# Performance work log

Hardware: AMD Instinct MI355X
Metric: run time of the kernel (lower is better)

The kernel has to match this reference:

```python
import jax, jax.numpy as jnp
import numpy as np

N = 100000       # num nodes
E = 1000000      # num edges
D_IN = 128       # input feature dim
D_H = 64         # hidden = output dim
EPS = 1e-5       # GraphNorm eps
SLOPE = 0.2      # LeakyReLU negative slope


def _glorot(key, shape):
    lim = float(np.sqrt(6.0 / (shape[0] + shape[1])))
    return jax.random.uniform(key, shape, jnp.float32, -lim, lim)


def setup_inputs() -> dict:
    key = jax.random.key(0)
    ks = jax.random.split(key, 6)
    return {
        "x": jax.random.normal(ks[0], (N, D_IN), jnp.float32),
        "edge_index": jax.random.randint(ks[1], (2, E), 0, N),
        "W_in": _glorot(ks[2], (D_IN, D_H)),
        "b_in": jnp.zeros((D_H,), jnp.float32),
        "W1": _glorot(ks[3], (D_H, D_H)),
        "b1": jnp.zeros((D_H,), jnp.float32),
        "gn1_alpha": jnp.ones((D_H,), jnp.float32),
        "gn1_gamma": jnp.ones((D_H,), jnp.float32),
        "gn1_beta": jnp.zeros((D_H,), jnp.float32),
        "W2": _glorot(ks[4], (D_H, D_H)),
        "b2": jnp.zeros((D_H,), jnp.float32),
        "gn2_alpha": jnp.ones((D_H,), jnp.float32),
        "gn2_gamma": jnp.ones((D_H,), jnp.float32),
        "gn2_beta": jnp.zeros((D_H,), jnp.float32),
    }


def gcn_conv(x, W, b, src, dst):
    # GCNConv with added self-loops and symmetric normalization:
    # out = D^{-1/2} (A + I) D^{-1/2} (x W) + b
    xw = x @ W                                                 # [N, D]
    ones = jnp.ones((src.shape[0],), x.dtype)
    deg = jax.ops.segment_sum(ones, dst, num_segments=x.shape[0]) + 1.0  # +1 self-loop
    dinv = jax.lax.rsqrt(deg)                                  # [N]
    coef = dinv[src] * dinv[dst]                               # [E]
    agg = jax.ops.segment_sum(xw[src] * coef[:, None], dst, num_segments=x.shape[0])
    return agg + xw * (dinv * dinv)[:, None] + b


def graph_norm(x, alpha, gamma, beta):
    # PyG GraphNorm over a single graph: per-feature mean/var over all nodes
    mean = jnp.mean(x, axis=0)
    c = x - alpha * mean
    var = jnp.mean(c * c, axis=0)
    return gamma * c * jax.lax.rsqrt(var + EPS) + beta


def reference(x, edge_index, W_in, b_in, W1, b1, gn1_alpha, gn1_gamma, gn1_beta,
              W2, b2, gn2_alpha, gn2_gamma, gn2_beta):
    src, dst = edge_index[0], edge_index[1]
    h = x @ W_in + b_in                                        # input projection
    h = graph_norm(gcn_conv(h, W1, b1, src, dst), gn1_alpha, gn1_gamma, gn1_beta)
    h = jnp.where(h > 0, h, SLOPE * h)                         # LeakyReLU(0.2); dropout=eval (identity)
    h = graph_norm(gcn_conv(h, W2, b2, src, dst), gn2_alpha, gn2_gamma, gn2_beta)
    return h                                                    # [N, D_H]
```

## Files before the change

kernel.cpp:

```cpp
#include <hip/hip_runtime.h>
#include <stdint.h>

#define N_NODES 100000
#define N_EDGES 1000000
#define D_IN 128
#define D_H 64
#define EPS 1e-5f
#define SLOPE 0.2f

typedef unsigned short u16;
typedef unsigned int u32;
typedef __attribute__((ext_vector_type(8))) short bf16x8;
typedef __attribute__((ext_vector_type(4))) float f32x4;

__device__ __forceinline__ float bf2f(u16 u) {
    union { u32 i; float f; } v; v.i = ((u32)u) << 16; return v.f;
}
__device__ __forceinline__ u16 f2bf(float f) {
    union { float f; u32 i; } v; v.f = f;
    u32 r = (v.i + 0x7fffu + ((v.i >> 16) & 1u)) >> 16;
    return (u16)r;
}
__device__ __forceinline__ bool is_f32(const void* flagp) {
    return *(const u32*)flagp == 0x3F800000u;
}
__device__ __forceinline__ float loadf(const void* p, size_t i, bool m) {
    return m ? ((const float*)p)[i] : bf2f(((const u16*)p)[i]);
}

__global__ __launch_bounds__(256) void kpf(const void* __restrict__ W_in,
                     const void* __restrict__ b_in,
                     const void* __restrict__ W1, const void* __restrict__ W2,
                     const void* __restrict__ flagp, const int* __restrict__ ei,
                     u16* __restrict__ WcT, u16* __restrict__ W2T,
                     float* __restrict__ bc, u16* __restrict__ xwb_pad,
                     int* __restrict__ cnt, int* __restrict__ bucket16,
                     int* __restrict__ ovf)
{
    bool m = is_f32(flagp);
    int t = threadIdx.x;
    int bid = blockIdx.x;
    if (bid < 64) {
        int c = bid;
        __shared__ float w1c[D_H];
        if (t < D_H) w1c[t] = loadf(W1, t * D_H + c, m);
        __syncthreads();
        if (t < D_IN) {
            float acc = 0.f;
            #pragma unroll 8
            for (int j = 0; j < D_H; j++) acc += loadf(W_in, t * D_H + j, m) * w1c[j];
            WcT[c * D_IN + t] = f2bf(acc);
        }
        if (t == 0) {
            float b = 0.f;
            for (int j = 0; j < D_H; j++) b += loadf(b_in, j, m) * w1c[j];
            bc[c] = b;
        }
        if (c == 0 && t < D_H) xwb_pad[(size_t)N_NODES * D_H + t] = 0;
    } else if (bid < 80) {
        int idx = (bid - 64) * 256 + t;
        int n = idx >> 6, k = idx & 63;
        W2T[n * D_H + k] = f2bf(loadf(W2, k * D_H + n, m));
    } else {
        int e4 = (bid - 80) * 1024 + t * 4;
        if (e4 < N_EDGES) {
            int4 s4 = *(const int4*)(ei + e4);
            int4 d4 = *(const int4*)(ei + N_EDGES + e4);
            int ss[4] = {s4.x, s4.y, s4.z, s4.w};
            int dd[4] = {d4.x, d4.y, d4.z, d4.w};
            #pragma unroll
            for (int j = 0; j < 4; j++) {
                int slot = atomicAdd(&cnt[dd[j]], 1);
                if (slot < 16)      bucket16[(size_t)dd[j] * 16 + slot] = ss[j];
                else if (slot < 64) ovf[(size_t)dd[j] * 48 + slot - 16] = ss[j];
            }
        }
    }
}

__global__ __launch_bounds__(256) void kgemm1(const void* __restrict__ x,
        const u16* __restrict__ WcT, const float* __restrict__ bc,
        const int* __restrict__ cnt, const void* __restrict__ flagp,
        u16* __restrict__ xwb)
{
    bool m = is_f32(flagp);
    __shared__ __align__(16) u16 xs[64 * 136];
    __shared__ __align__(16) u16 WT[64 * 136];
    int tid = threadIdx.x;
    int row0 = blockIdx.x * 64;
    for (int i = tid; i < 64 * 32; i += 256) {
        int r = i >> 5, kq = (i & 31) * 4;
        *(ushort4*)(WT + r * 136 + kq) = *(const ushort4*)(WcT + r * D_IN + kq);
    }
    for (int i = tid; i < 64 * 32; i += 256) {
        int r = i >> 5, kq = (i & 31) * 4;
        int gr = row0 + r;
        ushort4 u = make_ushort4(0, 0, 0, 0);
        if (gr < N_NODES) {
            if (m) {
                float4 v = *(const float4*)((const float*)x + (size_t)gr * D_IN + kq);
                u = make_ushort4(f2bf(v.x), f2bf(v.y), f2bf(v.z), f2bf(v.w));
            } else {
                u = *(const ushort4*)((const u16*)x + (size_t)gr * D_IN + kq);
            }
        }
        *(ushort4*)(xs + r * 136 + kq) = u;
    }
    __syncthreads();
    int w = tid >> 6, L = tid & 63;
    int q = L >> 4, c = L & 15;
    f32x4 acc[4];
    #pragma unroll
    for (int ct = 0; ct < 4; ct++) {
        float b = bc[ct * 16 + c];
        acc[ct] = (f32x4){b, b, b, b};
    }
    const u16* ap = xs + (w * 16 + c) * 136 + q * 8;
    #pragma unroll
    for (int kk = 0; kk < 4; kk++) {
        bf16x8 af = *(const bf16x8*)(ap + kk * 32);
        #pragma unroll
        for (int ct = 0; ct < 4; ct++) {
            bf16x8 bfr = *(const bf16x8*)(WT + (ct * 16 + c) * 136 + kk * 32 + q * 8);
            acc[ct] = __builtin_amdgcn_mfma_f32_16x16x32_bf16(af, bfr, acc[ct], 0, 0, 0);
        }
    }
    #pragma unroll
    for (int r = 0; r < 4; r++) {
        int gr = row0 + w * 16 + q * 4 + r;
        if (gr < N_NODES) {
            float ds = rsqrtf((float)cnt[gr] + 1.0f);
            #pragma unroll
            for (int ct = 0; ct < 4; ct++)
                xwb[(size_t)gr * D_H + ct * 16 + c] = f2bf(acc[ct][r] * ds);
        }
    }
}

__global__ __launch_bounds__(256) void kagg(const u16* __restrict__ xwb,
        const int* __restrict__ cnt, const int* __restrict__ bucket16,
        const int* __restrict__ ovf, const void* __restrict__ bvec,
        const void* __restrict__ flagp,
        u16* __restrict__ ybuf, float* __restrict__ accum)
{
    bool m = is_f32(flagp);
    __shared__ float red_s[4][64], red_q[4][64];
    int tid = threadIdx.x;
    int wv = tid >> 6, L = tid & 63;
    int half = L >> 5, mm = L & 31;
    int node0 = blockIdx.x * 32 + wv * 8;

    int cnt8 = cnt[node0 + (L & 7)];
    int tl = L >> 4, sl = L & 15;
    int raw0 = bucket16[(size_t)(node0 + tl) * 16 + sl];
    int raw1 = bucket16[(size_t)(node0 + 4 + tl) * 16 + sl];

    float b0 = loadf(bvec, 2 * mm, m), b1 = loadf(bvec, 2 * mm + 1, m);
    float ls0 = 0, ls1 = 0, lq0 = 0, lq1 = 0;

    const char* xb = (const char*)xwb;
    u32 moff = (u32)(mm << 2);

    auto srcof = [&](int g, int s, int degn, int ng) -> u32 {
        int rw = __shfl((g < 2) ? raw0 : raw1, (((g & 1) * 2 + half) << 4) + s);
        int sv = (s < degn) ? rw : ((s == degn) ? ng : N_NODES);
        return ((u32)sv << 7) | moff;
    };

    int cvg = __shfl(cnt8, half);
    int degn = min(cvg, 64);
    int ng = node0 + half;
    u32 cur[16];
    #pragma unroll
    for (int s = 0; s < 16; s++)
        cur[s] = *(const u32*)(xb + srcof(0, s, degn, ng));

    #pragma unroll
    for (int g = 0; g < 4; g++) {
        u32 nxt[16];
        int cvn = 0, degx = 0, ngx = 0;
        if (g < 3) {
            cvn = __shfl(cnt8, 2 * (g + 1) + half);
            degx = min(cvn, 64);
            ngx = node0 + 2 * (g + 1) + half;
            #pragma unroll
            for (int s = 0; s < 16; s++)
                nxt[s] = *(const u32*)(xb + srcof(g + 1, s, degx, ngx));
        }
        float a0 = 0.f, a1 = 0.f;
        #pragma unroll
        for (int s = 0; s < 16; s++) {
            a0 += __uint_as_float(cur[s] << 16);
            a1 += __uint_as_float(cur[s] & 0xffff0000u);
        }
        if (degn >= 16) {
            for (int s = 16; s <= degn; s++) {
                int sv = (s < degn) ? ovf[(size_t)ng * 48 + s - 16] : ng;
                u32 v = *(const u32*)(xb + (((u32)sv << 7) | moff));
                a0 += __uint_as_float(v << 16);
                a1 += __uint_as_float(v & 0xffff0000u);
            }
        }
        float ddn = rsqrtf((float)cvg + 1.0f);
        float y0 = ddn * a0 + b0;
        float y1 = ddn * a1 + b1;
        ((u32*)(ybuf + (size_t)ng * D_H))[mm] = (u32)f2bf(y0) | ((u32)f2bf(y1) << 16);
        ls0 += y0; ls1 += y1; lq0 += y0 * y0; lq1 += y1 * y1;
        #pragma unroll
        for (int s = 0; s < 16; s++) cur[s] = nxt[s];
        cvg = cvn; degn = degx; ng = ngx;
    }

    ls0 += __shfl_xor(ls0, 32); ls1 += __shfl_xor(ls1, 32);
    lq0 += __shfl_xor(lq0, 32); lq1 += __shfl_xor(lq1, 32);
    if (half == 0) {
        *(float2*)&red_s[wv][2 * mm] = make_float2(ls0, ls1);
        *(float2*)&red_q[wv][2 * mm] = make_float2(lq0, lq1);
    }
    __syncthreads();
    if (tid < 64) {
        atomicAdd(&accum[tid],      red_s[0][tid] + red_s[1][tid] + red_s[2][tid] + red_s[3][tid]);
        atomicAdd(&accum[64 + tid], red_q[0][tid] + red_q[1][tid] + red_q[2][tid] + red_q[3][tid]);
    }
}

__global__ __launch_bounds__(256) void kgemm2(const u16* __restrict__ y1b,
        const u16* __restrict__ W2T, const float* __restrict__ accum,
        const void* __restrict__ alpha, const void* __restrict__ gamma,
        const void* __restrict__ beta, const void* __restrict__ flagp,
        const int* __restrict__ cnt, u16* __restrict__ xwb)
{
    bool m = is_f32(flagp);
    __shared__ __align__(16) u16 hs[64 * 72];
    __shared__ __align__(16) u16 WT[64 * 72];
    __shared__ float aL[64], cL[64];
    int tid = threadIdx.x;
    if (tid < 64) {
        float mean = accum[tid] * (1.0f / N_NODES);
        float al = loadf(alpha, tid, m);
        float var = accum[64 + tid] * (1.0f / N_NODES) - mean * mean * al * (2.0f - al);
        var = fmaxf(var, 0.f);
        float a = loadf(gamma, tid, m) * rsqrtf(var + EPS);
        aL[tid] = a;
        cL[tid] = loadf(beta, tid, m) - a * al * mean;
    }
    for (int i = tid; i < 64 * 16; i += 256) {
        int r = i >> 4, kq = (i & 15) * 4;
        *(ushort4*)(WT + r * 72 + kq) = *(const ushort4*)(W2T + r * D_H + kq);
    }
    __syncthreads();
    int row0 = blockIdx.x * 64;
    for (int i = tid; i < 64 * 16; i += 256) {
        int r = i >> 4, kq = (i & 15) * 4;
        int gr = row0 + r;
        ushort4 u = make_ushort4(0, 0, 0, 0);
        if (gr < N_NODES) u = *(const ushort4*)(y1b + (size_t)gr * D_H + kq);
        float h0 = aL[kq + 0] * bf2f(u.x) + cL[kq + 0]; h0 = h0 > 0.f ? h0 : SLOPE * h0;
        float h1 = aL[kq + 1] * bf2f(u.y) + cL[kq + 1]; h1 = h1 > 0.f ? h1 : SLOPE * h1;
        float h2 = aL[kq + 2] * bf2f(u.z) + cL[kq + 2]; h2 = h2 > 0.f ? h2 : SLOPE * h2;
        float h3 = aL[kq + 3] * bf2f(u.w) + cL[kq + 3]; h3 = h3 > 0.f ? h3 : SLOPE * h3;
        *(ushort4*)(hs + r * 72 + kq) = make_ushort4(f2bf(h0), f2bf(h1), f2bf(h2), f2bf(h3));
    }
    __syncthreads();
    int w = tid >> 6, L = tid & 63;
    int q = L >> 4, c = L & 15;
    f32x4 acc[4] = {};
    const u16* ap = hs + (w * 16 + c) * 72 + q * 8;
    #pragma unroll
    for (int kk = 0; kk < 2; kk++) {
        bf16x8 af = *(const bf16x8*)(ap + kk * 32);
        #pragma unroll
        for (int ct = 0; ct < 4; ct++) {
            bf16x8 bfr = *(const bf16x8*)(WT + (ct * 16 + c) * 72 + kk * 32 + q * 8);
            acc[ct] = __builtin_amdgcn_mfma_f32_16x16x32_bf16(af, bfr, acc[ct], 0, 0, 0);
        }
    }
    #pragma unroll
    for (int r = 0; r < 4; r++) {
        int gr = row0 + w * 16 + q * 4 + r;
        if (gr < N_NODES) {
            float ds = rsqrtf((float)cnt[gr] + 1.0f);
            #pragma unroll
            for (int ct = 0; ct < 4; ct++)
                xwb[(size_t)gr * D_H + ct * 16 + c] = f2bf(acc[ct][r] * ds);
        }
    }
}

__global__ __launch_bounds__(256) void kout(const u16* __restrict__ y2b,
        const float* __restrict__ accum2, const void* __restrict__ alpha,
        const void* __restrict__ gamma, const void* __restrict__ beta,
        const void* __restrict__ flagp, void* __restrict__ out)
{
    bool m = is_f32(flagp);
    __shared__ float a2[64], c2[64];
    int tid = threadIdx.x;
    if (tid < 64) {
        float mean = accum2[tid] * (1.0f / N_NODES);
        float al = loadf(alpha, tid, m);
        float var = accum2[64 + tid] * (1.0f / N_NODES) - mean * mean * al * (2.0f - al);
        var = fmaxf(var, 0.f);
        float a = loadf(gamma, tid, m) * rsqrtf(var + EPS);
        a2[tid] = a;
        c2[tid] = loadf(beta, tid, m) - a * al * mean;
    }
    __syncthreads();
    int w0 = (blockIdx.x * 256 + tid) * 2;
    u32 v0 = ((const u32*)y2b)[w0];
    u32 v1 = ((const u32*)y2b)[w0 + 1];
    int f = (w0 * 2) & 63;
    float o0 = a2[f + 0] * __uint_as_float(v0 << 16)          + c2[f + 0];
    float o1 = a2[f + 1] * __uint_as_float(v0 & 0xffff0000u)  + c2[f + 1];
    float o2 = a2[f + 2] * __uint_as_float(v1 << 16)          + c2[f + 2];
    float o3 = a2[f + 3] * __uint_as_float(v1 & 0xffff0000u)  + c2[f + 3];
    if (m) {
        *(float4*)((float*)out + (size_t)w0 * 2) = make_float4(o0, o1, o2, o3);
    } else {
        u32 p0 = (u32)f2bf(o0) | ((u32)f2bf(o1) << 16);
        u32 p1 = (u32)f2bf(o2) | ((u32)f2bf(o3) << 16);
        *(uint2*)((u32*)out + w0) = make_uint2(p0, p1);
    }
}

extern "C" void kernel_launch(void* const* d_in, const int* in_sizes, int n_in,
                              void* d_out, int out_size, void* d_ws, size_t ws_size,
                              hipStream_t stream)
{
    const void* x    = d_in[0];
    const int*  ei   = (const int*)d_in[1];
    const void* W_in = d_in[2];
    const void* b_in = d_in[3];
    const void* W1   = d_in[4];
    const void* b1   = d_in[5];
    const void* gn1a = d_in[6];
    const void* gn1g = d_in[7];
    const void* gn1b = d_in[8];
    const void* W2   = d_in[9];
    const void* b2   = d_in[10];
    const void* gn2a = d_in[11];
    const void* gn2g = d_in[12];
    const void* gn2b = d_in[13];

    char* ws = (char*)d_ws;
    int*   cnt      = (int*)(ws + 0);
    float* accum    = (float*)(ws + 400000);
    float* bc       = (float*)(ws + 402048);
    u16*   WcT      = (u16*)(ws + 402432);
    u16*   W2T      = (u16*)(ws + 418816);
    int*   bucket16 = (int*)(ws + 1235200);
    int*   ovf      = (int*)(ws + 7635200);
    u16*   bufA     = (u16*)(ws + 26835200);
    u16*   bufB     = (u16*)(ws + 39635456);

    hipMemsetAsync(ws, 0, 400000 + 1024, stream);

    kpf<<<80 + (N_EDGES + 1023) / 1024, 256, 0, stream>>>(
        W_in, b_in, W1, W2, gn1a, ei, WcT, W2T, bc, bufA, cnt, bucket16, ovf);
    kgemm1<<<(N_NODES + 63) / 64, 256, 0, stream>>>(x, WcT, bc, cnt, gn1a, bufA);
    kagg<<<N_NODES / 32, 256, 0, stream>>>(bufA, cnt, bucket16, ovf, b1, gn1a,
                                           bufB, accum);
    kgemm2<<<(N_NODES + 63) / 64, 256, 0, stream>>>(bufB, W2T, accum, gn1a, gn1g,
                                                    gn1b, gn1a, cnt, bufA);
    kagg<<<N_NODES / 32, 256, 0, stream>>>(bufA, cnt, bucket16, ovf, b2, gn1a,
                                           bufB, accum + 128);
    kout<<<N_NODES * D_H / 1024, 256, 0, stream>>>(bufB, accum + 128, gn2a, gn2g,
                                                   gn2b, gn1a, d_out);
}
```

Baseline: 372.6 us.

## Move source-degree scaling into aggregation and overlap edge bucketing with first GEMM

The first GEMM used to depend on the degree counts, so edge bucketing and the x·W GEMM ran in separate launches. Source-side D^{-1/2} scaling now happens inside the aggregation kernel, using gathered per-edge rsqrt(cnt) values passed by shuffles. That removes the GEMM's dependency on cnt, and the bucketing blocks and the GEMM blocks are merged into one grid that runs concurrently. The cost is an extra random cnt gather per edge slot in both aggregation passes, plus an FMA in place of an add.

```diff
diff --git a/kernel.cpp b/kernel.cpp
--- a/kernel.cpp
+++ b/kernel.cpp
@@ -7,6 +7,7 @@
 #define D_H 64
 #define EPS 1e-5f
 #define SLOPE 0.2f
+#define N_EBLK ((N_EDGES + 1023) / 1024)
 
 typedef unsigned short u16;
 typedef unsigned int u32;
@@ -28,14 +29,11 @@
     return m ? ((const float*)p)[i] : bf2f(((const u16*)p)[i]);
 }
 
-__global__ __launch_bounds__(256) void kpf(const void* __restrict__ W_in,
-                     const void* __restrict__ b_in,
-                     const void* __restrict__ W1, const void* __restrict__ W2,
-                     const void* __restrict__ flagp, const int* __restrict__ ei,
-                     u16* __restrict__ WcT, u16* __restrict__ W2T,
-                     float* __restrict__ bc, u16* __restrict__ xwb_pad,
-                     int* __restrict__ cnt, int* __restrict__ bucket16,
-                     int* __restrict__ ovf)
+__global__ __launch_bounds__(256) void kprep(const void* __restrict__ W_in,
+        const void* __restrict__ b_in, const void* __restrict__ W1,
+        const void* __restrict__ W2, const void* __restrict__ flagp,
+        u16* __restrict__ WcT, u16* __restrict__ W2T,
+        float* __restrict__ bc, u16* __restrict__ xwb_pad)
 {
     bool m = is_f32(flagp);
     int t = threadIdx.x;
@@ -57,12 +55,22 @@
             bc[c] = b;
         }
         if (c == 0 && t < D_H) xwb_pad[(size_t)N_NODES * D_H + t] = 0;
-    } else if (bid < 80) {
+    } else {
         int idx = (bid - 64) * 256 + t;
         int n = idx >> 6, k = idx & 63;
         W2T[n * D_H + k] = f2bf(loadf(W2, k * D_H + n, m));
-    } else {
-        int e4 = (bid - 80) * 1024 + t * 4;
+    }
+}
+
+__global__ __launch_bounds__(256) void kmix(const void* __restrict__ x,
+        const u16* __restrict__ WcT, const float* __restrict__ bc,
+        const void* __restrict__ flagp, const int* __restrict__ ei,
+        u16* __restrict__ xwb, int* __restrict__ cnt,
+        int* __restrict__ bucket16, int* __restrict__ ovf)
+{
+    int tid = threadIdx.x;
+    if (blockIdx.x < N_EBLK) {
+        int e4 = blockIdx.x * 1024 + tid * 4;
         if (e4 < N_EDGES) {
             int4 s4 = *(const int4*)(ei + e4);
             int4 d4 = *(const int4*)(ei + N_EDGES + e4);
@@ -75,19 +83,12 @@
                 else if (slot < 64) ovf[(size_t)dd[j] * 48 + slot - 16] = ss[j];
             }
         }
-    }
-}
-
-__global__ __launch_bounds__(256) void kgemm1(const void* __restrict__ x,
-        const u16* __restrict__ WcT, const float* __restrict__ bc,
-        const int* __restrict__ cnt, const void* __restrict__ flagp,
-        u16* __restrict__ xwb)
-{
+        return;
+    }
     bool m = is_f32(flagp);
     __shared__ __align__(16) u16 xs[64 * 136];
     __shared__ __align__(16) u16 WT[64 * 136];
-    int tid = threadIdx.x;
-    int row0 = blockIdx.x * 64;
+    int row0 = (blockIdx.x - N_EBLK) * 64;
     for (int i = tid; i < 64 * 32; i += 256) {
         int r = i >> 5, kq = (i & 31) * 4;
         *(ushort4*)(WT + r * 136 + kq) = *(const ushort4*)(WcT + r * D_IN + kq);
@@ -129,10 +130,9 @@
     for (int r = 0; r < 4; r++) {
         int gr = row0 + w * 16 + q * 4 + r;
         if (gr < N_NODES) {
-            float ds = rsqrtf((float)cnt[gr] + 1.0f);
             #pragma unroll
             for (int ct = 0; ct < 4; ct++)
-                xwb[(size_t)gr * D_H + ct * 16 + c] = f2bf(acc[ct][r] * ds);
+                xwb[(size_t)gr * D_H + ct * 16 + c] = f2bf(acc[ct][r]);
         }
     }
 }
@@ -154,6 +154,13 @@
     int tl = L >> 4, sl = L & 15;
     int raw0 = bucket16[(size_t)(node0 + tl) * 16 + sl];
     int raw1 = bucket16[(size_t)(node0 + 4 + tl) * 16 + sl];
+
+    int deg0 = min(__shfl(cnt8, tl), 64);
+    int deg4 = min(__shfl(cnt8, 4 + tl), 64);
+    int s0i = sl < deg0 ? raw0 : node0 + tl;
+    int s1i = sl < deg4 ? raw1 : node0 + 4 + tl;
+    float ds0 = rsqrtf((float)cnt[s0i] + 1.0f);
+    float ds1 = rsqrtf((float)cnt[s1i] + 1.0f);
 
     float b0 = loadf(bvec, 2 * mm, m), b1 = loadf(bvec, 2 * mm + 1, m);
     float ls0 = 0, ls1 = 0, lq0 = 0, lq1 = 0;
@@ -190,15 +197,17 @@
         float a0 = 0.f, a1 = 0.f;
         #pragma unroll
         for (int s = 0; s < 16; s++) {
-            a0 += __uint_as_float(cur[s] << 16);
-            a1 += __uint_as_float(cur[s] & 0xffff0000u);
+            float sc = __shfl((g < 2) ? ds0 : ds1, (((g & 1) * 2 + half) << 4) + s);
+            a0 = fmaf(sc, __uint_as_float(cur[s] << 16), a0);
+            a1 = fmaf(sc, __uint_as_float(cur[s] & 0xffff0000u), a1);
         }
         if (degn >= 16) {
             for (int s = 16; s <= degn; s++) {
                 int sv = (s < degn) ? ovf[(size_t)ng * 48 + s - 16] : ng;
+                float sc = rsqrtf((float)cnt[sv] + 1.0f);
                 u32 v = *(const u32*)(xb + (((u32)sv << 7) | moff));
-                a0 += __uint_as_float(v << 16);
-                a1 += __uint_as_float(v & 0xffff0000u);
+                a0 = fmaf(sc, __uint_as_float(v << 16), a0);
+                a1 = fmaf(sc, __uint_as_float(v & 0xffff0000u), a1);
             }
         }
         float ddn = rsqrtf((float)cvg + 1.0f);
@@ -228,7 +237,7 @@
         const u16* __restrict__ W2T, const float* __restrict__ accum,
         const void* __restrict__ alpha, const void* __restrict__ gamma,
         const void* __restrict__ beta, const void* __restrict__ flagp,
-        const int* __restrict__ cnt, u16* __restrict__ xwb)
+        u16* __restrict__ xwb)
 {
     bool m = is_f32(flagp);
     __shared__ __align__(16) u16 hs[64 * 72];
@@ -279,10 +288,9 @@
     for (int r = 0; r < 4; r++) {
         int gr = row0 + w * 16 + q * 4 + r;
         if (gr < N_NODES) {
-            float ds = rsqrtf((float)cnt[gr] + 1.0f);
             #pragma unroll
             for (int ct = 0; ct < 4; ct++)
-                xwb[(size_t)gr * D_H + ct * 16 + c] = f2bf(acc[ct][r] * ds);
+                xwb[(size_t)gr * D_H + ct * 16 + c] = f2bf(acc[ct][r]);
         }
     }
 }
@@ -354,13 +362,13 @@
 
     hipMemsetAsync(ws, 0, 400000 + 1024, stream);
 
-    kpf<<<80 + (N_EDGES + 1023) / 1024, 256, 0, stream>>>(
-        W_in, b_in, W1, W2, gn1a, ei, WcT, W2T, bc, bufA, cnt, bucket16, ovf);
-    kgemm1<<<(N_NODES + 63) / 64, 256, 0, stream>>>(x, WcT, bc, cnt, gn1a, bufA);
+    kprep<<<80, 256, 0, stream>>>(W_in, b_in, W1, W2, gn1a, WcT, W2T, bc, bufA);
+    kmix<<<N_EBLK + (N_NODES + 63) / 64, 256, 0, stream>>>(
+        x, WcT, bc, gn1a, ei, bufA, cnt, bucket16, ovf);
     kagg<<<N_NODES / 32, 256, 0, stream>>>(bufA, cnt, bucket16, ovf, b1, gn1a,
                                            bufB, accum);
     kgemm2<<<(N_NODES + 63) / 64, 256, 0, stream>>>(bufB, W2T, accum, gn1a, gn1g,
-                                                    gn1b, gn1a, cnt, bufA);
+                                                    gn1b, gn1a, bufA);
     kagg<<<N_NODES / 32, 256, 0, stream>>>(bufA, cnt, bucket16, ovf, b2, gn1a,
                                            bufB, accum + 128);
     kout<<<N_NODES * D_H / 1024, 256, 0, stream>>>(bufB, accum + 128, gn2a, gn2g,
```

Result: slower. 404.0 us (+8.4%).
